# Kernel tuning notes

Measured on AMD Instinct MI355X. Metric: run time of the kernel, lower is better.

The kernel has to match this reference:

```python
import jax, jax.numpy as jnp
import numpy as np

NUM_PHRASE = 8
HDIM = 256
NUM_HEADS = 8
NUM_LAYERS = 3
MIN_DIST = 2


def sine_pos(mask, num_feats, temperature=10000.0):
    # PositionEmbeddingSine (1D, DETR-style, normalize=False)
    B, L = mask.shape
    x_embed = jnp.cumsum(mask.astype(jnp.float32), axis=1)            # [B,L]
    dim_t = jnp.arange(num_feats, dtype=jnp.float32)
    dim_t = temperature ** (2.0 * jnp.floor(dim_t / 2.0) / num_feats)
    pos = x_embed[:, :, None] / dim_t                                  # [B,L,C]
    pos = jnp.stack([jnp.sin(pos[:, :, 0::2]), jnp.cos(pos[:, :, 1::2])], axis=3)
    return pos.reshape(B, L, num_feats)


def layer_norm(x, g, b, eps=1e-5):
    mu = jnp.mean(x, axis=-1, keepdims=True)
    var = jnp.mean((x - mu) ** 2, axis=-1, keepdims=True)
    return (x - mu) / jnp.sqrt(var + eps) * g + b


def mha(q, k, v, key_mask, in_w, in_b, out_w, out_b, nheads):
    # torch nn.MultiheadAttention (batch_first, eval/no-dropout), averaged attn weights
    B, Lq, C = q.shape
    Dh = C // nheads
    qp = (q @ in_w[:, :C] + in_b[:C]).reshape(B, Lq, nheads, Dh)
    kp = (k @ in_w[:, C:2 * C] + in_b[C:2 * C]).reshape(B, -1, nheads, Dh)
    vp = (v @ in_w[:, 2 * C:] + in_b[2 * C:]).reshape(B, -1, nheads, Dh)
    scores = jnp.einsum('bqhd,bkhd->bhqk', qp, kp) / jnp.sqrt(jnp.float32(Dh))
    scores = jnp.where(key_mask[:, None, None, :], scores, -jnp.inf)
    attn = jax.nn.softmax(scores, axis=-1)
    out = jnp.einsum('bhqk,bkhd->bqhd', attn, vp).reshape(B, Lq, C)
    return out @ out_w + out_b, jnp.mean(attn, axis=1)


def cross_attention(x, y, mask, qw, qb, kvw, kvb, inw, inb, ow, ob, g0, b0, lw, lb, g1, b1):
    C = x.shape[-1]
    q = x @ qw + qb
    kv = y @ kvw + kvb
    k, v = kv[..., :C], kv[..., C:]
    q_att, attn = mha(q, k, v, mask, inw, inb, ow, ob, NUM_HEADS)
    x = layer_norm(x + q_att, g0, b0)
    update = jax.nn.relu(x @ lw + lb)
    x = layer_norm(x + update, g1, b1)
    return x, attn


def _select_one(entropy_b, mask_b):
    # greedy highest-entropy selection with min-distance suppression (1D NMS)
    P, MD = NUM_PHRASE, MIN_DIST
    score = jnp.where(mask_b, entropy_b, -jnp.inf)
    order = jnp.argsort(-score).astype(jnp.int32)   # valid indices first, descending entropy

    def step(carry, idx):
        sel, cnt = carry
        dists = jnp.where(sel >= 0, jnp.abs(idx - sel), 1000000)
        ok = mask_b[idx] & (cnt < P) & (jnp.min(dists) >= MD)
        new_sel = jnp.where(ok, sel.at[jnp.minimum(cnt, P - 1)].set(idx), sel)
        return (new_sel, cnt + ok.astype(jnp.int32)), None

    init = (jnp.full((P,), -1, jnp.int32), jnp.int32(0))
    (sel, cnt), _ = jax.lax.scan(step, init, order)
    last = sel[jnp.maximum(cnt - 1, 0)]
    return jnp.where(jnp.arange(P) < cnt, sel, last)   # pad by repeating last


def phrase_generate(txt_emb, txt_mask, video_feats, video_mask,
                    word_proj_w, word_proj_b, video_proj_w, video_proj_b,
                    q_w, q_b, kv_w, kv_b, in_w, in_b, out_w, out_b,
                    ln0_g, ln0_b, lin_w, lin_b, ln1_g, ln1_b, eos_slot):
    B, L, C = txt_emb.shape
    word_emb = txt_emb[:, 1:]
    word_mask = txt_mask[:, 1:]
    word_pe = word_emb + sine_pos(word_mask, C)

    # word importance via video cross-attention entropy
    wp = word_pe @ word_proj_w + word_proj_b                      # [B,Lw,C]
    vp = video_feats @ video_proj_w + video_proj_b                # [B,T,C]
    sim = jnp.einsum('blc,btc->blt', wp, vp)                      # [B,Lw,T]
    sim = jnp.where(video_mask[:, None, :], sim, -jnp.inf)
    attn_weights = jax.nn.softmax(sim, axis=2)
    entropy = -jnp.sum(attn_weights * jnp.log(attn_weights + 1e-6), axis=2)  # [B,Lw]

    sel = jax.vmap(_select_one)(entropy, word_mask)               # [B,P] int32
    phrase_slot = jnp.take_along_axis(word_pe, sel[:, :, None], axis=1)      # [B,P,C]

    slot_sim = None
    for i in range(NUM_LAYERS):
        phrase_slot, slot_sim = cross_attention(
            phrase_slot, word_pe, word_mask,
            q_w[i], q_b[i], kv_w[i], kv_b[i], in_w[i], in_b[i], out_w[i], out_b[i],
            ln0_g[i], ln0_b[i], lin_w[i], lin_b[i], ln1_g[i], ln1_b[i])

    eos = jnp.broadcast_to(eos_slot, (B, 1, C))
    return phrase_slot, attn_weights, slot_sim, eos


def setup_inputs() -> dict:
    key = jax.random.key(0)
    ks = jax.random.split(key, 16)
    B, L, T, C, NL = 128, 257, 1024, HDIM, NUM_LAYERS
    s = 0.02
    inp = {
        'txt_emb': jax.random.normal(ks[0], (B, L, C), jnp.float32),
        'txt_mask': jnp.ones((B, L), jnp.bool_),
        'video_feats': jax.random.normal(ks[1], (B, T, C), jnp.float32),
        'video_mask': jnp.ones((B, T), jnp.bool_),
        'word_proj_w': jax.random.normal(ks[2], (C, C)) * s,
        'word_proj_b': jnp.zeros((C,)),
        'video_proj_w': jax.random.normal(ks[3], (C, C)) * s,
        'video_proj_b': jnp.zeros((C,)),
        'q_w': jax.random.normal(ks[4], (NL, C, C)) * s,
        'q_b': jnp.zeros((NL, C)),
        'kv_w': jax.random.normal(ks[5], (NL, C, 2 * C)) * s,
        'kv_b': jnp.zeros((NL, 2 * C)),
        'in_w': jax.random.normal(ks[6], (NL, C, 3 * C)) * s,
        'in_b': jnp.zeros((NL, 3 * C)),
        'out_w': jax.random.normal(ks[7], (NL, C, C)) * s,
        'out_b': jnp.zeros((NL, C)),
        'ln0_g': jnp.ones((NL, C)),
        'ln0_b': jnp.zeros((NL, C)),
        'lin_w': jax.random.normal(ks[8], (NL, C, C)) * s,
        'lin_b': jnp.zeros((NL, C)),
        'ln1_g': jnp.ones((NL, C)),
        'ln1_b': jnp.zeros((NL, C)),
        'eos_slot': jax.random.normal(ks[9], (1, 1, C)),
    }
    return inp


def reference(txt_emb, txt_mask, video_feats, video_mask,
              word_proj_w, word_proj_b, video_proj_w, video_proj_b,
              q_w, q_b, kv_w, kv_b, in_w, in_b, out_w, out_b,
              ln0_g, ln0_b, lin_w, lin_b, ln1_g, ln1_b, eos_slot):
    return phrase_generate(txt_emb, txt_mask, video_feats, video_mask,
                           word_proj_w, word_proj_b, video_proj_w, video_proj_b,
                           q_w, q_b, kv_w, kv_b, in_w, in_b, out_w, out_b,
                           ln0_g, ln0_b, lin_w, lin_b, ln1_g, ln1_b, eos_slot)
```

## Files before the change

kernel.cpp:

```cpp
#include <hip/hip_runtime.h>
#include <math.h>

#define BB 128
#define LFULL 257
#define LW 256
#define TT 1024
#define CC 256
#define NH 8
#define DHD 32
#define PP 8
#define NLAY 3

typedef __bf16 bf16x8 __attribute__((ext_vector_type(8)));
typedef float  f32x4  __attribute__((ext_vector_type(4)));

__device__ __forceinline__ float blockReduceSum(float v, volatile float* lds) {
#pragma unroll
    for (int m = 32; m >= 1; m >>= 1) v += __shfl_xor(v, m);
    __syncthreads();
    if ((threadIdx.x & 63) == 0) lds[threadIdx.x >> 6] = v;
    __syncthreads();
    return lds[0] + lds[1] + lds[2] + lds[3];
}
__device__ __forceinline__ float blockReduceMax(float v, volatile float* lds) {
#pragma unroll
    for (int m = 32; m >= 1; m >>= 1) v = fmaxf(v, __shfl_xor(v, m));
    __syncthreads();
    if ((threadIdx.x & 63) == 0) lds[threadIdx.x >> 6] = v;
    __syncthreads();
    return fmaxf(fmaxf(lds[0], lds[1]), fmaxf(lds[2], lds[3]));
}

#define LP 40

template<int SPLIT, int B_F32, int OUT_SPLIT>
__global__ __launch_bounds__(256) void gemm_mfma(
    const __bf16* __restrict__ Ahi, const __bf16* __restrict__ Alo, int lda, long long sA,
    const void* __restrict__ Bhp, const void* __restrict__ Blp, int ldb, long long sB,
    const float* __restrict__ bias,
    float* __restrict__ Cf, __bf16* __restrict__ Chi, __bf16* __restrict__ Clo,
    int ldc, long long sC, int M, int N, int K)
{
    __shared__ __bf16 sAh[128 * LP];
    __shared__ __bf16 sAl[SPLIT ? 128 * LP : 1];
    __shared__ __bf16 sBh[128 * LP];
    __shared__ __bf16 sBl[SPLIT ? 128 * LP : 1];

    const int tid = threadIdx.x;
    const int n0 = blockIdx.x * 128;
    const int m0 = blockIdx.y * 128;
    const long long bz = blockIdx.z;
    const __bf16* Ah = Ahi + bz * sA;
    const __bf16* Al = SPLIT ? (Alo + bz * sA) : nullptr;

    const int wv = tid >> 6, lane = tid & 63;
    const int wm = (wv & 1) << 6, wn = (wv >> 1) << 6;
    const int lr = lane & 15, quad = lane >> 4;

    const int sr = tid >> 2;
    const int sc = (tid & 3) << 3;
    const int fr = tid >> 3;
    const int fc = (tid & 7) << 2;

    f32x4 acc[4][4];
#pragma unroll
    for (int i = 0; i < 4; ++i)
#pragma unroll
        for (int j = 0; j < 4; ++j) acc[i][j] = (f32x4)(0.f);

    for (int k0 = 0; k0 < K; k0 += 32) {
#pragma unroll
        for (int j = 0; j < 2; ++j) {
            int row = sr + 64 * j;
            *(bf16x8*)&sAh[row * LP + sc] =
                *(const bf16x8*)&Ah[(long long)(m0 + row) * lda + k0 + sc];
            if constexpr (SPLIT)
                *(bf16x8*)&sAl[row * LP + sc] =
                    *(const bf16x8*)&Al[(long long)(m0 + row) * lda + k0 + sc];
        }
        if constexpr (B_F32) {
            const float* Bf = (const float*)Bhp + bz * sB;
#pragma unroll
            for (int j = 0; j < 4; ++j) {
                int row = fr + 32 * j;
                float4 f = *(const float4*)&Bf[(long long)(n0 + row) * ldb + k0 + fc];
                __bf16 h0 = (__bf16)f.x, h1 = (__bf16)f.y, h2 = (__bf16)f.z, h3 = (__bf16)f.w;
                sBh[row * LP + fc + 0] = h0; sBh[row * LP + fc + 1] = h1;
                sBh[row * LP + fc + 2] = h2; sBh[row * LP + fc + 3] = h3;
                sBl[row * LP + fc + 0] = (__bf16)(f.x - (float)h0);
                sBl[row * LP + fc + 1] = (__bf16)(f.y - (float)h1);
                sBl[row * LP + fc + 2] = (__bf16)(f.z - (float)h2);
                sBl[row * LP + fc + 3] = (__bf16)(f.w - (float)h3);
            }
        } else {
            const __bf16* Bh = (const __bf16*)Bhp + bz * sB;
#pragma unroll
            for (int j = 0; j < 2; ++j) {
                int row = sr + 64 * j;
                *(bf16x8*)&sBh[row * LP + sc] =
                    *(const bf16x8*)&Bh[(long long)(n0 + row) * ldb + k0 + sc];
                if constexpr (SPLIT) {
                    const __bf16* Bl = (const __bf16*)Blp + bz * sB;
                    *(bf16x8*)&sBl[row * LP + sc] =
                        *(const bf16x8*)&Bl[(long long)(n0 + row) * ldb + k0 + sc];
                }
            }
        }
        __syncthreads();

        bf16x8 fah[4], fbh[4];
        bf16x8 fal[4], fbl[4];
#pragma unroll
        for (int i = 0; i < 4; ++i) {
            fah[i] = *(const bf16x8*)&sAh[(wm + i * 16 + lr) * LP + quad * 8];
            fbh[i] = *(const bf16x8*)&sBh[(wn + i * 16 + lr) * LP + quad * 8];
            if constexpr (SPLIT) {
                fal[i] = *(const bf16x8*)&sAl[(wm + i * 16 + lr) * LP + quad * 8];
                fbl[i] = *(const bf16x8*)&sBl[(wn + i * 16 + lr) * LP + quad * 8];
            }
        }
#pragma unroll
        for (int i = 0; i < 4; ++i)
#pragma unroll
            for (int j = 0; j < 4; ++j) {
                if constexpr (SPLIT) {
                    acc[i][j] = __builtin_amdgcn_mfma_f32_16x16x32_bf16(fal[i], fbh[j], acc[i][j], 0, 0, 0);
                    acc[i][j] = __builtin_amdgcn_mfma_f32_16x16x32_bf16(fah[i], fbl[j], acc[i][j], 0, 0, 0);
                }
                acc[i][j] = __builtin_amdgcn_mfma_f32_16x16x32_bf16(fah[i], fbh[j], acc[i][j], 0, 0, 0);
            }
        __syncthreads();
    }

#pragma unroll
    for (int i = 0; i < 4; ++i)
#pragma unroll
        for (int j = 0; j < 4; ++j) {
            int col = n0 + wn + j * 16 + lr;
            int row0 = m0 + wm + i * 16 + quad * 4;
            float bv = bias ? bias[col] : 0.f;
#pragma unroll
            for (int r = 0; r < 4; ++r) {
                float v = acc[i][j][r] + bv;
                long long off = (long long)(row0 + r) * ldc + col + bz * sC;
                if constexpr (OUT_SPLIT) {
                    __bf16 h = (__bf16)v;
                    Chi[off] = h;
                    Clo[off] = (__bf16)(v - (float)h);
                } else {
                    Cf[off] = v;
                }
            }
        }
}

#define GTS 64
#define GKT 16
#define GPAD 68

template<int TRANSB, int RELU, int TRANSC>
__global__ __launch_bounds__(256) void gemm_f32(
    const float* __restrict__ A, int lda, long long sA,
    const float* __restrict__ Bm, int ldb, long long sB,
    const float* __restrict__ bias,
    float* __restrict__ C, int ldc, long long sC,
    int M, int N, int K)
{
    __shared__ float As[GKT][GPAD];
    __shared__ float Bs[GKT][GPAD];
    const int tid = threadIdx.x;
    const int tx = tid & 15, ty = tid >> 4;
    const int n0 = blockIdx.x * GTS;
    const int m0 = blockIdx.y * GTS;
    const long long bz = blockIdx.z;
    const float* Ab = A + bz * sA;
    const float* Bb = Bm + bz * sB;
    float* Cb = C + bz * sC;

    const int lr = tid >> 2;
    const int lc = (tid & 3) << 2;
    const int br = tid >> 4;
    const int bc = (tid & 15) << 2;

    float acc[4][4] = {};

    for (int k0 = 0; k0 < K; k0 += GKT) {
        float4 a = *(const float4*)&Ab[(long long)(m0 + lr) * lda + k0 + lc];
        As[lc + 0][lr] = a.x; As[lc + 1][lr] = a.y;
        As[lc + 2][lr] = a.z; As[lc + 3][lr] = a.w;
        if (TRANSB) {
            float4 b = *(const float4*)&Bb[(long long)(n0 + lr) * ldb + k0 + lc];
            Bs[lc + 0][lr] = b.x; Bs[lc + 1][lr] = b.y;
            Bs[lc + 2][lr] = b.z; Bs[lc + 3][lr] = b.w;
        } else {
            float4 b = *(const float4*)&Bb[(long long)(k0 + br) * ldb + n0 + bc];
            *(float4*)&Bs[br][bc] = b;
        }
        __syncthreads();
#pragma unroll
        for (int k = 0; k < GKT; ++k) {
            float4 av = *(const float4*)&As[k][ty << 2];
            float4 bv = *(const float4*)&Bs[k][tx << 2];
            float ar[4] = {av.x, av.y, av.z, av.w};
            float brr[4] = {bv.x, bv.y, bv.z, bv.w};
#pragma unroll
            for (int i = 0; i < 4; ++i)
#pragma unroll
                for (int j = 0; j < 4; ++j)
                    acc[i][j] = fmaf(ar[i], brr[j], acc[i][j]);
        }
        __syncthreads();
    }

    float bbr[4] = {0.f, 0.f, 0.f, 0.f};
    if (bias) {
        float4 bb = *(const float4*)&bias[n0 + (tx << 2)];
        bbr[0] = bb.x; bbr[1] = bb.y; bbr[2] = bb.z; bbr[3] = bb.w;
    }
#pragma unroll
    for (int i = 0; i < 4; ++i) {
#pragma unroll
        for (int j = 0; j < 4; ++j) {
            float o = acc[i][j] + bbr[j];
            if (RELU) o = fmaxf(o, 0.f);
            if (TRANSC)
                Cb[(long long)(n0 + (tx << 2) + j) * ldc + m0 + (ty << 2) + i] = o;
            else
                Cb[(long long)(m0 + (ty << 2) + i) * ldc + n0 + (tx << 2) + j] = o;
        }
    }
}

__global__ __launch_bounds__(256) void word_pe_kernel(
    const float* __restrict__ te, const int* __restrict__ tm,
    __bf16* __restrict__ whi, __bf16* __restrict__ wlo)
{
    int b = blockIdx.x;
    int c = threadIdx.x;
    __shared__ float cums[LW];
    const int* m = tm + (long long)b * LFULL + 1;
    int s = 0;
    for (int i = 0; i <= c; ++i) s += (m[i] != 0);
    cums[c] = (float)s;
    __syncthreads();
    int i2 = c & ~1;
    float freq = powf(10000.0f, (float)i2 / (float)CC);
    const float* src = te + ((long long)b * LFULL + 1) * CC + c;
    long long base = (long long)b * LW * CC + c;
    for (int l = 0; l < LW; ++l) {
        float arg = cums[l] / freq;
        float pe = (c & 1) ? cosf(arg) : sinf(arg);
        float v = src[(long long)l * CC] + pe;
        __bf16 h = (__bf16)v;
        whi[base + (long long)l * CC] = h;
        wlo[base + (long long)l * CC] = (__bf16)(v - (float)h);
    }
}

__global__ __launch_bounds__(256) void split_transpose_kernel(
    const float* __restrict__ W, __bf16* __restrict__ hi, __bf16* __restrict__ lo)
{
    int n = blockIdx.x, k = threadIdx.x;
    float v = W[(long long)k * CC + n];
    __bf16 h = (__bf16)v;
    hi[(long long)n * CC + k] = h;
    lo[(long long)n * CC + k] = (__bf16)(v - (float)h);
}
__global__ __launch_bounds__(256) void split_plain_kernel(
    const float* __restrict__ W, __bf16* __restrict__ hi, __bf16* __restrict__ lo)
{
    int g = blockIdx.x * 256 + threadIdx.x;
    float v = W[g];
    __bf16 h = (__bf16)v;
    hi[g] = h;
    lo[g] = (__bf16)(v - (float)h);
}
__global__ __launch_bounds__(256) void cvt_bf16_kernel(
    const float* __restrict__ src, __bf16* __restrict__ dst)
{
    int g = blockIdx.x * 256 + threadIdx.x;
    dst[g] = (__bf16)src[g];
}

__global__ __launch_bounds__(256) void softmax_entropy_kernel(
    float* __restrict__ attn, const int* __restrict__ vmask,
    float* __restrict__ ent)
{
    __shared__ float lds[4];
    long long row = blockIdx.x;
    int b = blockIdx.x >> 8;
    float* p = attn + row * TT;
    const int* m = vmask + (long long)b * TT;
    int t4 = threadIdx.x * 4;
    float4 v = *(const float4*)&p[t4];
    int4 mm4 = *(const int4*)&m[t4];
    float x[4];
    x[0] = mm4.x ? v.x : -INFINITY;
    x[1] = mm4.y ? v.y : -INFINITY;
    x[2] = mm4.z ? v.z : -INFINITY;
    x[3] = mm4.w ? v.w : -INFINITY;
    float mx = fmaxf(fmaxf(x[0], x[1]), fmaxf(x[2], x[3]));
    mx = blockReduceMax(mx, lds);
    float e[4];
    float ps = 0.f;
#pragma unroll
    for (int j = 0; j < 4; ++j) { e[j] = expf(x[j] - mx); ps += e[j]; }
    float sum = blockReduceSum(ps, lds);
    float q[4];
    float ce = 0.f;
#pragma unroll
    for (int j = 0; j < 4; ++j) {
        q[j] = e[j] / sum;
        ce += q[j] * logf(q[j] + 1e-6f);
    }
    ce = blockReduceSum(ce, lds);
    *(float4*)&p[t4] = make_float4(q[0], q[1], q[2], q[3]);
    if (threadIdx.x == 0) ent[row] = -ce;
}

__global__ __launch_bounds__(256) void select_kernel(
    const float* __restrict__ ent, const int* __restrict__ tm,
    int* __restrict__ sel)
{
    int b = blockIdx.x;
    int l = threadIdx.x;
    __shared__ float sc[LW];
    __shared__ int ord[LW];
    __shared__ unsigned char mk[LW];
    mk[l] = (tm[(long long)b * LFULL + 1 + l] != 0);
    sc[l] = mk[l] ? ent[(long long)b * LW + l] : -INFINITY;
    __syncthreads();
    float mys = sc[l];
    int r = 0;
    for (int j = 0; j < LW; ++j) {
        float s = sc[j];
        r += (s > mys) || (s == mys && j < l);
    }
    ord[r] = l;
    __syncthreads();
    if (l == 0) {
        int chosen[PP];
        int cnt = 0;
        for (int t = 0; t < LW; ++t) {
            int idx = ord[t];
            if (!mk[idx]) continue;
            if (cnt >= PP) break;
            bool ok = true;
            for (int s2 = 0; s2 < cnt; ++s2) {
                int d = idx - chosen[s2];
                if (d < 0) d = -d;
                if (d < 2) ok = false;
            }
            if (ok) chosen[cnt++] = idx;
        }
        int last = (cnt > 0) ? chosen[cnt - 1] : -1;
        for (int p = 0; p < PP; ++p)
            sel[b * PP + p] = (p < cnt) ? chosen[p] : last;
    }
}

__global__ __launch_bounds__(256) void gather_kernel(
    const __bf16* __restrict__ whi, const __bf16* __restrict__ wlo,
    const int* __restrict__ sel, float* __restrict__ x0)
{
    int g = blockIdx.x * 256 + threadIdx.x;
    int b = g >> 11;
    int p = (g >> 8) & 7;
    int c = g & 255;
    int idx = sel[b * PP + p];
    if (idx < 0) idx = 0;
    long long off = ((long long)b * LW + idx) * CC + c;
    x0[g] = (float)whi[off] + (float)wlo[off];
}

__global__ __launch_bounds__(256) void eff_bias_kernel(
    const float* __restrict__ q_b, const float* __restrict__ kv_b,
    const float* __restrict__ in_w, const float* __restrict__ in_b,
    float* __restrict__ BQE_all, float* __restrict__ bkv3)
{
    int i = blockIdx.x / 3;
    int role = blockIdx.x % 3;
    int n = threadIdx.x;
    const float* inw = in_w + (long long)i * 196608;
    const float* inb = in_b + (long long)i * 768;
    const float* srcb;
    int co;
    float* dst;
    if (role == 0)      { srcb = q_b + i * 256;        co = 0;   dst = BQE_all + i * 256; }
    else if (role == 1) { srcb = kv_b + i * 512;       co = 256; dst = bkv3 + i * 512; }
    else                { srcb = kv_b + i * 512 + 256; co = 512; dst = bkv3 + i * 512 + 256; }
    float s = inb[co + n];
    for (int k = 0; k < CC; ++k)
        s = fmaf(srcb[k], inw[(long long)k * 768 + co + n], s);
    dst[n] = s;
}

__global__ __launch_bounds__(256) void attn_scores_kernel(
    const float* __restrict__ qp, const float* __restrict__ KV,
    const int* __restrict__ tm, float* __restrict__ attn)
{
    int b = blockIdx.x, h = blockIdx.y;
    int tid = threadIdx.x;
    __shared__ float qs[PP][DHD];
    __shared__ float sc[PP][LW];
    __shared__ float mxs[PP], sms[PP];
    {
        int q = tid >> 5, d = tid & 31;
        qs[q][d] = qp[((long long)(b * PP + q)) * CC + h * DHD + d];
    }
    __syncthreads();
    const float* kr = KV + ((long long)(b * LW + tid)) * 512 + h * DHD;
    float kreg[DHD];
#pragma unroll
    for (int j = 0; j < 8; ++j) {
        float4 f = *(const float4*)&kr[j * 4];
        kreg[j * 4 + 0] = f.x; kreg[j * 4 + 1] = f.y;
        kreg[j * 4 + 2] = f.z; kreg[j * 4 + 3] = f.w;
    }
    bool mk = tm[(long long)b * LFULL + 1 + tid] != 0;
#pragma unroll
    for (int q = 0; q < PP; ++q) {
        float s = 0.f;
#pragma unroll
        for (int d = 0; d < DHD; ++d) s = fmaf(qs[q][d], kreg[d], s);
        sc[q][tid] = mk ? s * 0.17677669529663687f : -INFINITY;
    }
    __syncthreads();
    {
        int q = tid >> 5, j = tid & 31;
        float m = -INFINITY;
        for (int kk = j; kk < LW; kk += 32) m = fmaxf(m, sc[q][kk]);
#pragma unroll
        for (int mm = 16; mm >= 1; mm >>= 1) m = fmaxf(m, __shfl_xor(m, mm, 32));
        float s = 0.f;
        for (int kk = j; kk < LW; kk += 32) s += expf(sc[q][kk] - m);
#pragma unroll
        for (int mm = 16; mm >= 1; mm >>= 1) s += __shfl_xor(s, mm, 32);
        if (j == 0) { mxs[q] = m; sms[q] = s; }
    }
    __syncthreads();
#pragma unroll
    for (int q = 0; q < PP; ++q) {
        float pv = expf(sc[q][tid] - mxs[q]) / sms[q];
        attn[(((long long)(b * NH + h)) * PP + q) * LW + tid] = pv;
    }
}

__global__ __launch_bounds__(256) void attn_out_kernel(
    const float* __restrict__ attn, const float* __restrict__ KV,
    float* __restrict__ aout)
{
    int b = blockIdx.x, q = blockIdx.y;
    int c = threadIdx.x, h = c >> 5;
    __shared__ float att[NH][LW];
#pragma unroll
    for (int hh = 0; hh < NH; ++hh)
        att[hh][c] = attn[(((long long)(b * NH + hh)) * PP + q) * LW + c];
    __syncthreads();
    const float* vpb = KV + ((long long)b * LW) * 512 + 256 + c;
    float acc = 0.f;
#pragma unroll 8
    for (int k = 0; k < LW; ++k)
        acc = fmaf(att[h][k], vpb[(long long)k * 512], acc);
    aout[((long long)(b * PP + q)) * CC + c] = acc;
}

__global__ __launch_bounds__(256) void slot_sim_kernel(
    const float* __restrict__ attn, float* __restrict__ outs)
{
    int b = blockIdx.x, q = blockIdx.y, k = threadIdx.x;
    float s = 0.f;
#pragma unroll
    for (int h = 0; h < NH; ++h)
        s += attn[(((long long)(b * NH + h)) * PP + q) * LW + k];
    outs[((long long)(b * PP + q)) * LW + k] = s * 0.125f;
}

__global__ __launch_bounds__(256) void ln_residual_kernel(
    const float* __restrict__ xin, const float* __restrict__ add,
    const float* __restrict__ g, const float* __restrict__ bta,
    float* __restrict__ out)
{
    __shared__ float lds[4];
    int r = blockIdx.x, c = threadIdx.x;
    long long idx = (long long)r * CC + c;
    float v = xin[idx] + add[idx];
    float s = blockReduceSum(v, lds);
    float mu = s * (1.0f / (float)CC);
    float d = v - mu;
    float var = blockReduceSum(d * d, lds) * (1.0f / (float)CC);
    out[idx] = d / sqrtf(var + 1e-5f) * g[c] + bta[c];
}

__global__ __launch_bounds__(256) void eos_kernel(
    const float* __restrict__ eos, float* __restrict__ outp)
{
    outp[(long long)blockIdx.x * CC + threadIdx.x] = eos[threadIdx.x];
}

extern "C" void kernel_launch(void* const* d_in, const int* in_sizes, int n_in,
                              void* d_out, int out_size, void* d_ws, size_t ws_size,
                              hipStream_t stream) {
    const float* txt_emb     = (const float*)d_in[0];
    const int*   txt_mask    = (const int*)d_in[1];
    const float* video_feats = (const float*)d_in[2];
    const int*   video_mask  = (const int*)d_in[3];
    const float* word_proj_w = (const float*)d_in[4];
    const float* word_proj_b = (const float*)d_in[5];
    const float* video_proj_w = (const float*)d_in[6];
    const float* q_w   = (const float*)d_in[8];
    const float* q_b   = (const float*)d_in[9];
    const float* kv_w  = (const float*)d_in[10];
    const float* kv_b  = (const float*)d_in[11];
    const float* in_w  = (const float*)d_in[12];
    const float* in_b  = (const float*)d_in[13];
    const float* out_w = (const float*)d_in[14];
    const float* out_b = (const float*)d_in[15];
    const float* ln0_g = (const float*)d_in[16];
    const float* ln0_b = (const float*)d_in[17];
    const float* lin_w = (const float*)d_in[18];
    const float* lin_b = (const float*)d_in[19];
    const float* ln1_g = (const float*)d_in[20];
    const float* ln1_b = (const float*)d_in[21];
    const float* eos_slot = (const float*)d_in[22];

    float* ws = (float*)d_ws;
    __bf16* wpe_hi = (__bf16*)(ws + 0LL);
    __bf16* wpe_lo = (__bf16*)(ws + 4194304LL);
    __bf16* wp_hi  = (__bf16*)(ws + 8388608LL);
    __bf16* wp_lo  = (__bf16*)(ws + 12582912LL);
    __bf16* U_hi   = (__bf16*)(ws + 16777216LL);
    __bf16* U_lo   = (__bf16*)(ws + 20971520LL);
    float*  KV     = ws + 8388608LL;
    float* ent     = ws + 25165824LL;
    int*   sel     = (int*)(ws + 25198592LL);
    float* x0      = ws + 25199616LL;
    float* x1      = ws + 25461760LL;
    float* xmid    = ws + 25723904LL;
    float* qp      = ws + 25986048LL;
    float* attnw   = ws + 26248192LL;
    float* aout    = ws + 28345344LL;
    float* qatt    = ws + 28607488LL;
    float* upd     = ws + 28869632LL;
    float* WQE_all = ws + 29131776LL;
    float* BQE_all = ws + 29328384LL;
    float* WT3f    = ws + 29329152LL;
    __bf16* WT3    = (__bf16*)(ws + 29722368LL);
    float* bkv3    = ws + 29918976LL;
    __bf16* WPT_hi = (__bf16*)(ws + 29920512LL);
    __bf16* WPT_lo = (__bf16*)(ws + 29953280LL);
    __bf16* VPS_hi = (__bf16*)(ws + 29986048LL);
    __bf16* VPS_lo = (__bf16*)(ws + 30018816LL);

    float* outp     = (float*)d_out;
    float* out_ps   = outp;
    float* out_attn = outp + 262144LL;
    float* out_slot = outp + 33816576LL;
    float* out_eos  = outp + 34078720LL;

    word_pe_kernel<<<dim3(BB), dim3(256), 0, stream>>>(txt_emb, txt_mask, wpe_hi, wpe_lo);
    split_transpose_kernel<<<dim3(256), dim3(256), 0, stream>>>(word_proj_w, WPT_hi, WPT_lo);
    split_plain_kernel<<<dim3(256), dim3(256), 0, stream>>>(video_proj_w, VPS_hi, VPS_lo);
    gemm_mfma<1,0,1><<<dim3(2,256,1), dim3(256), 0, stream>>>(
        wpe_hi, wpe_lo, 256, 0, WPT_hi, WPT_lo, 256, 0, word_proj_b,
        nullptr, wp_hi, wp_lo, 256, 0, 32768, 256, 256);
    gemm_mfma<1,0,1><<<dim3(2,256,1), dim3(256), 0, stream>>>(
        wp_hi, wp_lo, 256, 0, VPS_hi, VPS_lo, 256, 0, nullptr,
        nullptr, U_hi, U_lo, 256, 0, 32768, 256, 256);
    gemm_mfma<1,1,0><<<dim3(8,2,BB), dim3(256), 0, stream>>>(
        U_hi, U_lo, 256, 65536LL, video_feats, nullptr, 256, 262144LL, nullptr,
        out_attn, nullptr, nullptr, 1024, 262144LL, 256, 1024, 256);
    softmax_entropy_kernel<<<dim3(32768), dim3(256), 0, stream>>>(out_attn, video_mask, ent);
    select_kernel<<<dim3(BB), dim3(256), 0, stream>>>(ent, txt_mask, sel);
    gather_kernel<<<dim3(1024), dim3(256), 0, stream>>>(wpe_hi, wpe_lo, sel, x0);

    gemm_f32<0,0,0><<<dim3(4,4,3), dim3(256), 0, stream>>>(
        q_w,256,65536LL, in_w,768,196608LL, nullptr, WQE_all,256,65536LL, 256,256,256);
    gemm_f32<0,0,1><<<dim3(4,4,3), dim3(256), 0, stream>>>(
        kv_w,512,131072LL, in_w+256,768,196608LL, nullptr, WT3f,256,131072LL, 256,256,256);
    gemm_f32<0,0,1><<<dim3(4,4,3), dim3(256), 0, stream>>>(
        kv_w+256,512,131072LL, in_w+512,768,196608LL, nullptr, WT3f+65536,256,131072LL, 256,256,256);
    eff_bias_kernel<<<dim3(9), dim3(256), 0, stream>>>(q_b, kv_b, in_w, in_b, BQE_all, bkv3);
    cvt_bf16_kernel<<<dim3(1536), dim3(256), 0, stream>>>(WT3f, (__bf16*)WT3);

    float* X = x0;
    for (int i = 0; i < NLAY; ++i) {
        const float* ow  = out_w + (long long)i * 65536;
        const float* ob  = out_b + (long long)i * 256;
        const float* g0  = ln0_g + (long long)i * 256;
        const float* b0  = ln0_b + (long long)i * 256;
        const float* lw  = lin_w + (long long)i * 65536;
        const float* lb  = lin_b + (long long)i * 256;
        const float* g1  = ln1_g + (long long)i * 256;
        const float* b1  = ln1_b + (long long)i * 256;

        gemm_mfma<0,0,0><<<dim3(4,256,1), dim3(256), 0, stream>>>(
            wpe_hi, nullptr, 256, 0, WT3 + (long long)i * 131072, nullptr, 256, 0,
            bkv3 + i * 512, KV, nullptr, nullptr, 512, 0, 32768, 512, 256);

        gemm_f32<0,0,0><<<dim3(4,16,1), dim3(256), 0, stream>>>(
            X,256,0, WQE_all + (long long)i*65536,256,0, BQE_all + i*256, qp,256,0, 1024,256,256);

        attn_scores_kernel<<<dim3(BB,NH), dim3(256), 0, stream>>>(qp, KV, txt_mask, attnw);
        attn_out_kernel<<<dim3(BB,PP), dim3(256), 0, stream>>>(attnw, KV, aout);
        if (i == NLAY - 1)
            slot_sim_kernel<<<dim3(BB,PP), dim3(256), 0, stream>>>(attnw, out_slot);

        gemm_f32<0,0,0><<<dim3(4,16,1), dim3(256), 0, stream>>>(
            aout,256,0, ow,256,0, ob, qatt,256,0, 1024,256,256);
        ln_residual_kernel<<<dim3(1024), dim3(256), 0, stream>>>(X, qatt, g0, b0, xmid);
        gemm_f32<0,1,0><<<dim3(4,16,1), dim3(256), 0, stream>>>(
            xmid,256,0, lw,256,0, lb, upd,256,0, 1024,256,256);
        float* Xout = (i == NLAY - 1) ? out_ps : ((X == x0) ? x1 : x0);
        ln_residual_kernel<<<dim3(1024), dim3(256), 0, stream>>>(xmid, upd, g1, b1, Xout);
        X = Xout;
    }
    eos_kernel<<<dim3(BB), dim3(256), 0, stream>>>(eos_slot, out_eos);
}
```

Measured before the change: 1.068 ms.

## Split word positional embedding into scan, PE table, and vectorized add kernels

Replaces the per-batch word_pe_kernel, which used 128 blocks, a quadratic serial cumsum and per-element sin/cos, with three kernels. The first does a wave-shuffle prefix scan of the mask. The second builds a 257-row sin/cos table indexed by count. The third is a wide, float4-vectorized kernel that adds the looked-up table row and splits the sum into bf16 hi/lo parts. This removes the low-parallelism, transcendental-heavy loop at the cost of two extra launches and reads of a small table. The workspace slots used for cums and petab are assumed to be free.

```diff
diff --git a/kernel.cpp b/kernel.cpp
--- a/kernel.cpp
+++ b/kernel.cpp
@@ -12,6 +12,7 @@
 #define NLAY 3
 
 typedef __bf16 bf16x8 __attribute__((ext_vector_type(8)));
+typedef __bf16 bf16x4 __attribute__((ext_vector_type(4)));
 typedef float  f32x4  __attribute__((ext_vector_type(4)));
 
 __device__ __forceinline__ float blockReduceSum(float v, volatile float* lds) {
@@ -231,30 +232,57 @@
     }
 }
 
-__global__ __launch_bounds__(256) void word_pe_kernel(
-    const float* __restrict__ te, const int* __restrict__ tm,
-    __bf16* __restrict__ whi, __bf16* __restrict__ wlo)
-{
-    int b = blockIdx.x;
+
+__global__ __launch_bounds__(256) void cumsum_kernel(
+    const int* __restrict__ tm, int* __restrict__ cums)
+{
+    int b = blockIdx.x, c = threadIdx.x;
+    int lane = c & 63;
+    int v = (tm[(long long)b * LFULL + 1 + c] != 0) ? 1 : 0;
+#pragma unroll
+    for (int off = 1; off < 64; off <<= 1) {
+        int t = __shfl_up(v, off);
+        if (lane >= off) v += t;
+    }
+    __shared__ int wsum[4];
+    if (lane == 63) wsum[c >> 6] = v;
+    __syncthreads();
+    int w = c >> 6, add = 0;
+    for (int i = 0; i < w; ++i) add += wsum[i];
+    cums[b * LW + c] = v + add;
+}
+
+__global__ __launch_bounds__(256) void pe_table_kernel(float* __restrict__ petab)
+{
+    int n = blockIdx.x;
     int c = threadIdx.x;
-    __shared__ float cums[LW];
-    const int* m = tm + (long long)b * LFULL + 1;
-    int s = 0;
-    for (int i = 0; i <= c; ++i) s += (m[i] != 0);
-    cums[c] = (float)s;
-    __syncthreads();
     int i2 = c & ~1;
     float freq = powf(10000.0f, (float)i2 / (float)CC);
-    const float* src = te + ((long long)b * LFULL + 1) * CC + c;
-    long long base = (long long)b * LW * CC + c;
-    for (int l = 0; l < LW; ++l) {
-        float arg = cums[l] / freq;
-        float pe = (c & 1) ? cosf(arg) : sinf(arg);
-        float v = src[(long long)l * CC] + pe;
-        __bf16 h = (__bf16)v;
-        whi[base + (long long)l * CC] = h;
-        wlo[base + (long long)l * CC] = (__bf16)(v - (float)h);
-    }
+    float arg = (float)n / freq;
+    petab[n * CC + c] = (c & 1) ? cosf(arg) : sinf(arg);
+}
+
+__global__ __launch_bounds__(256) void word_pe2_kernel(
+    const float* __restrict__ te, const int* __restrict__ cums,
+    const float* __restrict__ petab,
+    __bf16* __restrict__ whi, __bf16* __restrict__ wlo)
+{
+    int g = blockIdx.x * 256 + threadIdx.x;
+    int c0 = (g & 63) << 2;
+    int l  = (g >> 6) & 255;
+    int b  = g >> 14;
+    int cnt = cums[b * LW + l];
+    float4 s = *(const float4*)&te[((long long)(b * LFULL + 1 + l)) * CC + c0];
+    float4 p = *(const float4*)&petab[cnt * CC + c0];
+    float v0 = s.x + p.x, v1 = s.y + p.y, v2 = s.z + p.z, v3 = s.w + p.w;
+    bf16x4 h, lo;
+    h[0] = (__bf16)v0; lo[0] = (__bf16)(v0 - (float)h[0]);
+    h[1] = (__bf16)v1; lo[1] = (__bf16)(v1 - (float)h[1]);
+    h[2] = (__bf16)v2; lo[2] = (__bf16)(v2 - (float)h[2]);
+    h[3] = (__bf16)v3; lo[3] = (__bf16)(v3 - (float)h[3]);
+    long long o = ((long long)(b * LW + l)) * CC + c0;
+    *(bf16x4*)&whi[o] = h;
+    *(bf16x4*)&wlo[o] = lo;
 }
 
 __global__ __launch_bounds__(256) void split_transpose_kernel(
@@ -552,13 +580,18 @@
     __bf16* VPS_hi = (__bf16*)(ws + 29986048LL);
     __bf16* VPS_lo = (__bf16*)(ws + 30018816LL);
 
+    int*   cums  = (int*)(ws + 8388608LL);
+    float* petab = ws + 8421376LL;
+
     float* outp     = (float*)d_out;
     float* out_ps   = outp;
     float* out_attn = outp + 262144LL;
     float* out_slot = outp + 33816576LL;
     float* out_eos  = outp + 34078720LL;
 
-    word_pe_kernel<<<dim3(BB), dim3(256), 0, stream>>>(txt_emb, txt_mask, wpe_hi, wpe_lo);
+    cumsum_kernel<<<dim3(BB), dim3(256), 0, stream>>>(txt_mask, cums);
+    pe_table_kernel<<<dim3(257), dim3(256), 0, stream>>>(petab);
+    word_pe2_kernel<<<dim3(8192), dim3(256), 0, stream>>>(txt_emb, cums, petab, wpe_hi, wpe_lo);
     split_transpose_kernel<<<dim3(256), dim3(256), 0, stream>>>(word_proj_w, WPT_hi, WPT_lo);
     split_plain_kernel<<<dim3(256), dim3(256), 0, stream>>>(video_proj_w, VPS_hi, VPS_lo);
     gemm_mfma<1,0,1><<<dim3(2,256,1), dim3(256), 0, stream>>>(
```

Measured after the change: 907.4 us. -15.0%, faster.
